# Optimization experiments

Hardware: AMD Instinct MI355X
Metric: run time of the kernel (lower is better)

The kernel has to match this reference:

```python
import jax, jax.numpy as jnp
import numpy as np

NC = 80            # num_classes
REG_MAX = 16
STRIDES = (8, 16, 32)
IMG = 640.0
TOPK = 10
TAL_ALPHA = 0.5
TAL_BETA = 6.0
L_BOX, L_CLS, L_DFL = 7.5, 0.5, 1.5
EPS = 1e-9
NEG = -1e8


def bbox_iou(b1, b2, ciou=False, eps=1e-7):
    # b1, b2: (..., 4) xyxy, broadcastable
    inter_wh = jnp.clip(jnp.minimum(b1[..., 2:], b2[..., 2:]) - jnp.maximum(b1[..., :2], b2[..., :2]), 0.0)
    inter = inter_wh[..., 0] * inter_wh[..., 1]
    w1 = jnp.clip(b1[..., 2] - b1[..., 0], 0.0); h1 = jnp.clip(b1[..., 3] - b1[..., 1], 0.0)
    w2 = jnp.clip(b2[..., 2] - b2[..., 0], 0.0); h2 = jnp.clip(b2[..., 3] - b2[..., 1], 0.0)
    union = w1 * h1 + w2 * h2 - inter + eps
    iou = inter / union
    if not ciou:
        return iou
    cx1 = (b1[..., 0] + b1[..., 2]) * 0.5; cy1 = (b1[..., 1] + b1[..., 3]) * 0.5
    cx2 = (b2[..., 0] + b2[..., 2]) * 0.5; cy2 = (b2[..., 1] + b2[..., 3]) * 0.5
    rho2 = (cx2 - cx1) ** 2 + (cy2 - cy1) ** 2
    cw = jnp.maximum(b1[..., 2], b2[..., 2]) - jnp.minimum(b1[..., 0], b2[..., 0])
    ch = jnp.maximum(b1[..., 3], b2[..., 3]) - jnp.minimum(b1[..., 1], b2[..., 1])
    c2 = cw ** 2 + ch ** 2 + eps
    v = (4.0 / np.pi ** 2) * (jnp.arctan(w2 / (h2 + eps)) - jnp.arctan(w1 / (h1 + eps))) ** 2
    alpha = jax.lax.stop_gradient(v / (1.0 - iou + v + eps))  # torch computes alpha under no_grad
    return iou - (rho2 / c2 + alpha * v)


def _assign_one(pred_scores, pred_bboxes, anchor_points, gt_labels, gt_bboxes):
    """TaskAlignedAssigner for one image.
    pred_scores (N,nc), pred_bboxes (N,4), anchor_points (N,2), gt_labels (M,), gt_bboxes (M,4).
    Returns target_bboxes (N,4), target_scores (N,nc), fg_mask (N,)."""
    N = pred_bboxes.shape[0]; M = gt_bboxes.shape[0]
    gl = jnp.clip(gt_labels.astype(jnp.int32), 0, NC - 1)
    x = anchor_points[:, 0]; y = anchor_points[:, 1]
    l = x[:, None] - gt_bboxes[None, :, 0]
    t = y[:, None] - gt_bboxes[None, :, 1]
    r = gt_bboxes[None, :, 2] - x[:, None]
    b = gt_bboxes[None, :, 3] - y[:, None]
    in_gts = (l > 0) & (t > 0) & (r > 0) & (b > 0)                     # (N,M)
    ious = bbox_iou(pred_bboxes[:, None, :], gt_bboxes[None, :, :])    # (N,M)
    cls_score = pred_scores[:, gl]                                     # (N,M)
    align = jnp.clip(cls_score, 0.0) ** TAL_ALPHA * jnp.clip(ious, 0.0) ** TAL_BETA
    align = jnp.where(in_gts, align, NEG)
    k = min(TOPK, N)
    _, topk_idx = jax.lax.top_k(align.T, k)                            # (M,k) indices into N
    mask_topk = jnp.zeros((M, N), dtype=bool).at[jnp.arange(M)[:, None], topk_idx].set(True).T
    mask_pos = mask_topk & in_gts                                      # (N,M)
    ious_pos = jnp.where(mask_pos, ious, -1.0)
    max_iou = ious_pos.max(axis=1)
    gt_idx = ious_pos.argmax(axis=1)                                   # (N,)
    fg_mask = max_iou > -0.5
    metric_pos = jnp.where(mask_pos, align, NEG)
    metric_max = jnp.clip(metric_pos.max(axis=0), EPS)                 # (M,)
    rows = jnp.arange(N)
    score = align[rows, gt_idx] / metric_max[gt_idx] * ious[rows, gt_idx]
    score = jnp.clip(score, 0.0, 1.0) * fg_mask.astype(pred_scores.dtype)
    tcls = gl[gt_idx]
    target_scores = jnp.zeros((N, NC), dtype=pred_scores.dtype).at[rows, tcls].set(score)
    target_bboxes = jnp.where(fg_mask[:, None], gt_bboxes[gt_idx], 0.0)
    return target_bboxes, target_scores, fg_mask


def _df_loss(reg_logits, target):
    # reg_logits (B,N,4,R) logits, target (B,N,4) float in [0,R-1] -> (B,N)
    t = jnp.clip(target, 0.0, float(REG_MAX - 1))
    left = jnp.floor(t).astype(jnp.int32)
    right = jnp.minimum(left + 1, REG_MAX - 1)
    wl = right.astype(t.dtype) - t
    wr = t - left.astype(t.dtype)
    same = right == left
    wl = jnp.where(same, 1.0, wl)
    wr = jnp.where(same, 0.0, wr)
    logp = jax.nn.log_softmax(reg_logits, axis=-1)
    ll = -jnp.take_along_axis(logp, left[..., None], axis=-1)[..., 0]
    lr = -jnp.take_along_axis(logp, right[..., None], axis=-1)[..., 0]
    return (ll * wl + lr * wr).sum(axis=-1)


def _forward(p0, p1, p2, gt_bboxes, gt_labels):
    preds = [p0, p1, p2]
    B = p0.shape[0]
    reg_ch = 4 * REG_MAX
    cls_list, reg_list, ap_list, st_list = [], [], [], []
    for p, s in zip(preds, STRIDES):
        _, _, h, w = p.shape
        reg = p[:, :reg_ch]
        cls = p[:, reg_ch:]
        cls_list.append(cls.transpose(0, 2, 3, 1).reshape(B, -1, NC))
        reg_list.append(reg.transpose(0, 2, 3, 1).reshape(B, -1, 4, REG_MAX))
        gy, gx = jnp.meshgrid(jnp.arange(h), jnp.arange(w), indexing='ij')
        pts = jnp.stack([(gx + 0.5) * s, (gy + 0.5) * s], axis=-1).reshape(-1, 2).astype(p.dtype)
        ap_list.append(pts)
        st_list.append(jnp.full((h * w,), float(s), dtype=p.dtype))
    cls_logits = jnp.concatenate(cls_list, axis=1)      # (B,N,nc)
    reg_logits = jnp.concatenate(reg_list, axis=1)      # (B,N,4,R)
    anchor_points = jnp.concatenate(ap_list, axis=0)    # (N,2)
    stride_t = jnp.concatenate(st_list, axis=0)         # (N,)
    pred_scores = jax.nn.sigmoid(cls_logits)
    proj = jnp.arange(REG_MAX, dtype=cls_logits.dtype)
    dist = (jax.nn.softmax(reg_logits, axis=-1) * proj).sum(-1) * stride_t[None, :, None]  # (B,N,4)
    ax = anchor_points[:, 0]; ay = anchor_points[:, 1]
    pred_bboxes = jnp.stack([ax - dist[..., 0], ay - dist[..., 1], ax + dist[..., 2], ay + dist[..., 3]], axis=-1)
    # --- TAL assignment (runs under no_grad in torch) ---
    tb, ts, fg = jax.vmap(lambda ps, pb, gl, gb: _assign_one(ps, pb, anchor_points, gl, gb))(
        jax.lax.stop_gradient(pred_scores), jax.lax.stop_gradient(pred_bboxes), gt_labels, gt_bboxes)
    tb = jax.lax.stop_gradient(tb)
    ts = jax.lax.stop_gradient(ts)
    ts_sum = jnp.maximum(ts.sum(), 1.0)
    # --- cls: BCE with logits over all anchors/classes ---
    z = cls_logits
    bce = jnp.clip(z, 0.0) - z * ts + jnp.log1p(jnp.exp(-jnp.abs(z)))
    loss_cls = bce.sum() / ts_sum
    # --- box: CIoU weighted by target score, fg only ---
    weight = ts.sum(-1) * fg.astype(ts.dtype)           # (B,N)
    ciou = bbox_iou(pred_bboxes, tb, ciou=True)         # (B,N)
    loss_box = ((1.0 - ciou) * weight).sum() / ts_sum
    # --- dfl ---
    inv_s = 1.0 / stride_t
    tl = (ax - tb[..., 0]) * inv_s
    tt = (ay - tb[..., 1]) * inv_s
    tr = (tb[..., 2] - ax) * inv_s
    tbm = (tb[..., 3] - ay) * inv_s
    target_ltrb = jnp.clip(jnp.stack([tl, tt, tr, tbm], axis=-1), 0.0, float(REG_MAX - 1))
    dfl = _df_loss(reg_logits, target_ltrb)             # (B,N)
    loss_dfl = (dfl * weight).sum() / ts_sum
    return L_BOX * loss_box + L_CLS * loss_cls + L_DFL * loss_dfl


def setup_inputs() -> dict:
    key = jax.random.key(0)
    k0, k1, k2, kc, kw, kl = jax.random.split(key, 6)
    B, C = 16, 4 * REG_MAX + NC
    p0 = jax.random.normal(k0, (B, C, 80, 80), dtype=jnp.float32)
    p1 = jax.random.normal(k1, (B, C, 40, 40), dtype=jnp.float32)
    p2 = jax.random.normal(k2, (B, C, 20, 20), dtype=jnp.float32)
    M = 32
    cxy = jax.random.uniform(kc, (B, M, 2), minval=64.0, maxval=IMG - 64.0)
    wh = jax.random.uniform(kw, (B, M, 2), minval=16.0, maxval=128.0)
    gt_bboxes = jnp.concatenate([cxy - wh * 0.5, cxy + wh * 0.5], axis=-1).astype(jnp.float32)
    gt_labels = jax.random.randint(kl, (B, M), 0, NC, dtype=jnp.int32).astype(jnp.int64)
    return {"p0": p0, "p1": p1, "p2": p2, "gt_bboxes": gt_bboxes, "gt_labels": gt_labels}


def reference(p0, p1, p2, gt_bboxes, gt_labels):
    return _forward(p0, p1, p2, gt_bboxes, gt_labels)
```

## Files before the change

### kernel.cpp

```cpp
#include <hip/hip_runtime.h>

#define BATCH 16
#define NANCH 8400
#define MGT 32
#define NCLS 80
#define RCH 64
#define NCH 144
#define TOPKK 10
#define MAXC 576
#define TKB 512
#define DECB 2100
#define BCEB 2625
#define TOTB (TKB + DECB + BCEB)
#define FINB 525

struct AInfo { int lvl, pos, W, HW; float s, ax, ay; };

__device__ __forceinline__ AInfo anchor_of(int n) {
  AInfo a;
  if (n < 6400)      { a.lvl = 0; a.pos = n;        a.W = 80; a.HW = 6400; a.s = 8.f;  }
  else if (n < 8000) { a.lvl = 1; a.pos = n - 6400; a.W = 40; a.HW = 1600; a.s = 16.f; }
  else               { a.lvl = 2; a.pos = n - 8000; a.W = 20; a.HW = 400;  a.s = 32.f; }
  int px = a.pos % a.W, py = a.pos / a.W;
  a.ax = (px + 0.5f) * a.s;
  a.ay = (py + 0.5f) * a.s;
  return a;
}

__device__ __forceinline__ const float* lvl_ptr(const float* p0, const float* p1,
                                                const float* p2, int lvl) {
  return lvl == 0 ? p0 : (lvl == 1 ? p1 : p2);
}

__device__ __forceinline__ float4 decode_box(const float* __restrict__ p, size_t chbase,
                                             int HW, float s, float ax, float ay) {
  float d[4];
  #pragma unroll
  for (int q = 0; q < 4; ++q) {
    float z[16]; float zm = -1e30f;
    #pragma unroll
    for (int j = 0; j < 16; ++j) {
      z[j] = p[chbase + (size_t)(q * 16 + j) * HW];
      zm = fmaxf(zm, z[j]);
    }
    float se = 0.f, ae = 0.f;
    #pragma unroll
    for (int j = 0; j < 16; ++j) {
      float e = __expf(z[j] - zm);
      se += e; ae += e * (float)j;
    }
    d[q] = ae / se * s;
  }
  return make_float4(ax - d[0], ay - d[1], ax + d[2], ay + d[3]);
}

__device__ __forceinline__ float iou_xyxy(float4 a, float4 b) {
  float ix = fmaxf(fminf(a.z, b.z) - fmaxf(a.x, b.x), 0.f);
  float iy = fmaxf(fminf(a.w, b.w) - fmaxf(a.y, b.y), 0.f);
  float inter = ix * iy;
  float w1 = fmaxf(a.z - a.x, 0.f), h1 = fmaxf(a.w - a.y, 0.f);
  float w2 = fmaxf(b.z - b.x, 0.f), h2 = fmaxf(b.w - b.y, 0.f);
  float uni = w1 * h1 + w2 * h2 - inter + 1e-7f;
  return inter / uni;
}

__device__ __forceinline__ float ciou_xyxy(float4 a, float4 b) {
  const float eps = 1e-7f;
  float ix = fmaxf(fminf(a.z, b.z) - fmaxf(a.x, b.x), 0.f);
  float iy = fmaxf(fminf(a.w, b.w) - fmaxf(a.y, b.y), 0.f);
  float inter = ix * iy;
  float w1 = fmaxf(a.z - a.x, 0.f), h1 = fmaxf(a.w - a.y, 0.f);
  float w2 = fmaxf(b.z - b.x, 0.f), h2 = fmaxf(b.w - b.y, 0.f);
  float uni = w1 * h1 + w2 * h2 - inter + eps;
  float iou = inter / uni;
  float cx1 = (a.x + a.z) * 0.5f, cy1 = (a.y + a.w) * 0.5f;
  float cx2 = (b.x + b.z) * 0.5f, cy2 = (b.y + b.w) * 0.5f;
  float rho2 = (cx2 - cx1) * (cx2 - cx1) + (cy2 - cy1) * (cy2 - cy1);
  float cw = fmaxf(a.z, b.z) - fminf(a.x, b.x);
  float ch = fmaxf(a.w, b.w) - fminf(a.y, b.y);
  float c2 = cw * cw + ch * ch + eps;
  const float kpi = 4.f / (float)(M_PI * M_PI);
  float dat = atanf(w2 / (h2 + eps)) - atanf(w1 / (h1 + eps));
  float v = kpi * dat * dat;
  float alpha = v / (1.f - iou + v + eps);
  return iou - (rho2 / c2 + alpha * v);
}

__device__ __forceinline__ float block_sum256(float v) {
  __shared__ float sm[4];
  #pragma unroll
  for (int off = 32; off; off >>= 1) v += __shfl_xor(v, off);
  __syncthreads();
  if ((threadIdx.x & 63) == 0) sm[threadIdx.x >> 6] = v;
  __syncthreads();
  return (threadIdx.x == 0) ? (sm[0] + sm[1] + sm[2] + sm[3]) : 0.f;
}

__device__ __forceinline__ double block_sum256d(double v) {
  __shared__ double smd[4];
  #pragma unroll
  for (int off = 32; off; off >>= 1) v += __shfl_xor(v, off);
  __syncthreads();
  if ((threadIdx.x & 63) == 0) smd[threadIdx.x >> 6] = v;
  __syncthreads();
  return (threadIdx.x == 0) ? (smd[0] + smd[1] + smd[2] + smd[3]) : 0.0;
}

__global__ __launch_bounds__(256) void k_one(
    const float* __restrict__ p0, const float* __restrict__ p1, const float* __restrict__ p2,
    const float* __restrict__ gtb, const int* __restrict__ gtl,
    float* __restrict__ pboxf, float* __restrict__ logz,
    float* __restrict__ metric_max, unsigned long long* __restrict__ slots,
    float* __restrict__ bce_part) {
  __shared__ float val[MAXC];
  __shared__ int   idx[MAXC];
  __shared__ float cio[MAXC];
  __shared__ float rv[4];
  __shared__ int   ri[4], rs[4], sdone[1];
  int blk = blockIdx.x, tid = threadIdx.x;

  if (blk >= TKB + DECB) {
    int r = blk - (TKB + DECB);
    int i = r * 256 + tid;
    float lb = 0.f;
    #pragma unroll
    for (int j = 0; j < 4; ++j) {
      int u = i + j * 672000;
      int b = u / 168000;
      int rr = u % 168000;
      const float4* src;
      if (rr < 128000)      src = (const float4*)p0 + ((size_t)(b * NCH + RCH) * 1600 + rr);
      else if (rr < 160000) src = (const float4*)p1 + ((size_t)(b * NCH + RCH) * 400 + (rr - 128000));
      else                  src = (const float4*)p2 + ((size_t)(b * NCH + RCH) * 100 + (rr - 160000));
      float4 z4 = *src;
      lb += fmaxf(z4.x, 0.f) + __logf(1.f + __expf(-fabsf(z4.x)));
      lb += fmaxf(z4.y, 0.f) + __logf(1.f + __expf(-fabsf(z4.y)));
      lb += fmaxf(z4.z, 0.f) + __logf(1.f + __expf(-fabsf(z4.z)));
      lb += fmaxf(z4.w, 0.f) + __logf(1.f + __expf(-fabsf(z4.w)));
    }
    float tot = block_sum256(lb);
    if (tid == 0) bce_part[r] = tot;
    return;
  }

  if (blk >= TKB) {
    int db = blk - TKB;
    int q = db & 3;
    int i = (db >> 2) * 256 + tid;
    int b = i / NANCH, n = i % NANCH;
    AInfo A = anchor_of(n);
    const float* p = lvl_ptr(p0, p1, p2, A.lvl);
    size_t base = (size_t)b * NCH * A.HW + A.pos;

    float z[16]; float zm = -1e30f;
    #pragma unroll
    for (int j = 0; j < 16; ++j) {
      z[j] = p[base + (size_t)(q * 16 + j) * A.HW];
      zm = fmaxf(zm, z[j]);
    }
    float se = 0.f, ae = 0.f;
    #pragma unroll
    for (int j = 0; j < 16; ++j) {
      float e = __expf(z[j] - zm);
      se += e; ae += e * (float)j;
    }
    float d = ae / se * A.s;
    float v = (q == 0) ? A.ax - d : (q == 1) ? A.ay - d : (q == 2) ? A.ax + d : A.ay + d;
    pboxf[(size_t)i * 4 + q] = v;
    logz[(size_t)i * 4 + q] = zm + __logf(se);
    return;
  }

  int b = blk >> 5, m = blk & 31;
  float4 g = ((const float4*)gtb)[b * MGT + m];
  int gl = min(max(gtl[b * MGT + m], 0), NCLS - 1);

  const int   Ws[3] = {80, 40, 20};
  const float ss[3] = {8.f, 16.f, 32.f};
  const int   nb[3] = {0, 6400, 8000};
  int x0[3], y0[3], nxl[3], cb[3];
  int cnt = 0;
  #pragma unroll
  for (int L = 0; L < 3; ++L) {
    float s = ss[L]; int W = Ws[L];
    int ax0 = max((int)floorf(g.x / s - 0.5f), 0);
    int ax1 = min((int)ceilf (g.z / s - 0.5f), W - 1);
    int ay0 = max((int)floorf(g.y / s - 0.5f), 0);
    int ay1 = min((int)ceilf (g.w / s - 0.5f), W - 1);
    int nx = max(ax1 - ax0 + 1, 0);
    int ny = max(ay1 - ay0 + 1, 0);
    x0[L] = ax0; y0[L] = ay0; nxl[L] = nx;
    cb[L] = cnt; cnt += nx * ny;
  }
  int C = min(cnt, MAXC);

  for (int t = tid; t < C; t += 256) {
    int L = (t >= cb[2]) ? 2 : (t >= cb[1]) ? 1 : 0;
    int r = t - cb[L];
    int ix = r % nxl[L], iy = r / nxl[L];
    int px = x0[L] + ix, py = y0[L] + iy;
    float ax = (px + 0.5f) * ss[L], ay = (py + 0.5f) * ss[L];
    float al = -3e38f, iou = 0.f; int n = 0x7fffffff;
    if (ax > g.x && ay > g.y && ax < g.z && ay < g.w) {
      int W = Ws[L];
      int HW = (L == 0) ? 6400 : (L == 1) ? 1600 : 400;
      int pos = py * W + px;
      n = nb[L] + pos;
      const float* p = lvl_ptr(p0, p1, p2, L);
      size_t chbase = (size_t)b * NCH * HW + pos;
      float4 pb = decode_box(p, chbase, HW, ss[L], ax, ay);
      iou = iou_xyxy(pb, g);
      float z = p[chbase + (size_t)(RCH + gl) * HW];
      float sg = 1.f / (1.f + __expf(-z));
      float i3 = iou * iou * iou;
      al = sqrtf(sg) * i3 * i3;
    }
    val[t] = al; idx[t] = n; cio[t] = iou;
  }
  __syncthreads();

  float mmax = -1.f;
  for (int k = 0; k < TOPKK; ++k) {
    float bv = -3e38f; int bn = 0x7fffffff, bs = 0;
    for (int t = tid; t < C; t += 256) {
      float v = val[t]; int n2 = idx[t];
      if (v > bv || (v == bv && n2 < bn)) { bv = v; bn = n2; bs = t; }
    }
    #pragma unroll
    for (int off = 32; off; off >>= 1) {
      float ov = __shfl_xor(bv, off);
      int   on = __shfl_xor(bn, off);
      int   os = __shfl_xor(bs, off);
      if (ov > bv || (ov == bv && on < bn)) { bv = ov; bn = on; bs = os; }
    }
    if ((tid & 63) == 0) { rv[tid >> 6] = bv; ri[tid >> 6] = bn; rs[tid >> 6] = bs; }
    __syncthreads();
    if (tid == 0) {
      #pragma unroll
      for (int w = 1; w < 4; ++w)
        if (rv[w] > bv || (rv[w] == bv && ri[w] < bn)) { bv = rv[w]; bn = ri[w]; bs = rs[w]; }
      if (bv >= 0.f) {
        mmax = fmaxf(mmax, bv);
        unsigned long long key = (1ULL << 62) |
                                 ((unsigned long long)__float_as_uint(cio[bs]) << 6) |
                                 (unsigned long long)(31 - m);
        atomicMax(&slots[(size_t)b * NANCH + bn], key);
        val[bs] = -3e38f;
        sdone[0] = 0;
      } else sdone[0] = 1;
    }
    __syncthreads();
    if (sdone[0]) break;
  }
  if (tid == 0) metric_max[b * MGT + m] = fmaxf(mmax, 1e-9f);
}

__global__ __launch_bounds__(256) void k_fin(
    const float* __restrict__ p0, const float* __restrict__ p1, const float* __restrict__ p2,
    const float4* __restrict__ pbox, const float* __restrict__ logz,
    const float* __restrict__ gtb, const int* __restrict__ gtl,
    const float* __restrict__ metric_max, const unsigned long long* __restrict__ slots,
    float4* __restrict__ fin_part) {
  int i = blockIdx.x * 256 + threadIdx.x;
  unsigned long long key = slots[i];
  float ts_p = 0.f, zc_p = 0.f, box_p = 0.f, dfl_p = 0.f;
  if (key) {
    int b = i / NANCH, n = i % NANCH;
    int m = 31 - (int)(key & 63ULL);
    float iou = __uint_as_float((unsigned int)((key >> 6) & 0xFFFFFFFFULL));
    AInfo A = anchor_of(n);
    float4 g = ((const float4*)gtb)[b * MGT + m];
    int gl = min(max(gtl[b * MGT + m], 0), NCLS - 1);
    const float* p = lvl_ptr(p0, p1, p2, A.lvl);
    size_t base = (size_t)b * NCH * A.HW + A.pos;

    float z = p[base + (size_t)(RCH + gl) * A.HW];
    float sg = 1.f / (1.f + __expf(-z));
    float i3 = iou * iou * iou;
    float align = sqrtf(sg) * i3 * i3;
    float mm = metric_max[b * MGT + m];
    float score = fminf(fmaxf(align / mm * iou, 0.f), 1.f);

    ts_p = score;
    zc_p = z * score;

    float4 pb = pbox[i];
    float ciou = ciou_xyxy(pb, g);
    box_p = (1.f - ciou) * score;

    float4 lz4 = ((const float4*)logz)[i];
    float inv_s = 1.f / A.s;
    float targ0 = (A.ax - g.x) * inv_s;
    float targ1 = (A.ay - g.y) * inv_s;
    float targ2 = (g.z - A.ax) * inv_s;
    float targ3 = (g.w - A.ay) * inv_s;
    float dfl = 0.f;
    #pragma unroll
    for (int sd = 0; sd < 4; ++sd) {
      float tg = sd == 0 ? targ0 : sd == 1 ? targ1 : sd == 2 ? targ2 : targ3;
      float lZ = sd == 0 ? lz4.x : sd == 1 ? lz4.y : sd == 2 ? lz4.z : lz4.w;
      float t = fminf(fmaxf(tg, 0.f), 15.f);
      int left = (int)floorf(t);
      int right = min(left + 1, 15);
      float wl, wr;
      if (right == left) { wl = 1.f; wr = 0.f; }
      else               { wl = (float)right - t; wr = t - (float)left; }
      float zl = p[base + (size_t)(sd * 16 + left)  * A.HW];
      float zr = p[base + (size_t)(sd * 16 + right) * A.HW];
      dfl += wl * (lZ - zl) + wr * (lZ - zr);
    }
    dfl_p = dfl * score;
  }
  float s0 = block_sum256(box_p);
  float s1 = block_sum256(zc_p);
  float s2 = block_sum256(dfl_p);
  float s3 = block_sum256(ts_p);
  if (threadIdx.x == 0) fin_part[blockIdx.x] = make_float4(s0, s1, s2, s3);
}

__global__ void k_out(const float* __restrict__ bce_part, const float4* __restrict__ fin_part,
                      float* __restrict__ out) {
  int tid = threadIdx.x;
  double sb = 0.0, s0 = 0.0, s1 = 0.0, s2 = 0.0, s3 = 0.0;
  for (int t = tid; t < BCEB; t += 256) sb += (double)bce_part[t];
  for (int t = tid; t < FINB; t += 256) {
    float4 f = fin_part[t];
    s0 += (double)f.x; s1 += (double)f.y; s2 += (double)f.z; s3 += (double)f.w;
  }
  sb = block_sum256d(sb);
  s0 = block_sum256d(s0);
  s1 = block_sum256d(s1);
  s2 = block_sum256d(s2);
  s3 = block_sum256d(s3);
  if (tid == 0) {
    double ts = fmax(s3, 1.0);
    out[0] = (float)(7.5 * s0 / ts + 0.5 * (sb - s1) / ts + 1.5 * s2 / ts);
  }
}

extern "C" void kernel_launch(void* const* d_in, const int* in_sizes, int n_in,
                              void* d_out, int out_size, void* d_ws, size_t ws_size,
                              hipStream_t stream) {
  const float* p0  = (const float*)d_in[0];
  const float* p1  = (const float*)d_in[1];
  const float* p2  = (const float*)d_in[2];
  const float* gtb = (const float*)d_in[3];
  const int*   gtl = (const int*)d_in[4];
  float* out = (float*)d_out;

  char* ws = (char*)d_ws;
  float*  metric_max = (float*)ws;
  float*  bce_part   = (float*)(ws + 2048);
  float4* fin_part   = (float4*)(ws + 12560);
  float*  pboxf      = (float*)(ws + 20960);
  float4* pbox       = (float4*)(ws + 20960);
  float*  logz       = (float*)(ws + 2171360);
  unsigned long long* slots = (unsigned long long*)(ws + 4321760);

  hipMemsetAsync(slots, 0, (size_t)BATCH * NANCH * 8, stream);
  k_one<<<TOTB, 256, 0, stream>>>(p0, p1, p2, gtb, gtl, pboxf, logz,
                                  metric_max, slots, bce_part);
  k_fin<<<FINB, 256, 0, stream>>>(p0, p1, p2, pbox, logz, gtb, gtl,
                                  metric_max, slots, fin_part);
  k_out<<<1, 256, 0, stream>>>(bce_part, fin_part, out);
}
```

Measured before the change: 135.3 us.

## Decode DFL boxes only for foreground anchors inside the final kernel

Removes the dense decode pass that computed softmax-expected box distances and log-partition values for every anchor and wrote them to workspace. The final kernel now recomputes these only for anchors that received an assignment, reading all 64 regression logits per foreground anchor. This drops a large read of the regression channels plus the pbox/logz writes and reads. In exchange, foreground threads do more gathered loads, and warps are divergent because only some lanes are foreground.

```diff
diff --git a/kernel.cpp b/kernel.cpp
--- a/kernel.cpp
+++ b/kernel.cpp
@@ -9,9 +9,8 @@
 #define TOPKK 10
 #define MAXC 576
 #define TKB 512
-#define DECB 2100
 #define BCEB 2625
-#define TOTB (TKB + DECB + BCEB)
+#define TOTB (TKB + BCEB)
 #define FINB 525
 
 struct AInfo { int lvl, pos, W, HW; float s, ax, ay; };
@@ -109,7 +108,6 @@
 __global__ __launch_bounds__(256) void k_one(
     const float* __restrict__ p0, const float* __restrict__ p1, const float* __restrict__ p2,
     const float* __restrict__ gtb, const int* __restrict__ gtl,
-    float* __restrict__ pboxf, float* __restrict__ logz,
     float* __restrict__ metric_max, unsigned long long* __restrict__ slots,
     float* __restrict__ bce_part) {
   __shared__ float val[MAXC];
@@ -119,8 +117,8 @@
   __shared__ int   ri[4], rs[4], sdone[1];
   int blk = blockIdx.x, tid = threadIdx.x;
 
-  if (blk >= TKB + DECB) {
-    int r = blk - (TKB + DECB);
+  if (blk >= TKB) {
+    int r = blk - TKB;
     int i = r * 256 + tid;
     float lb = 0.f;
     #pragma unroll
@@ -140,34 +138,6 @@
     }
     float tot = block_sum256(lb);
     if (tid == 0) bce_part[r] = tot;
-    return;
-  }
-
-  if (blk >= TKB) {
-    int db = blk - TKB;
-    int q = db & 3;
-    int i = (db >> 2) * 256 + tid;
-    int b = i / NANCH, n = i % NANCH;
-    AInfo A = anchor_of(n);
-    const float* p = lvl_ptr(p0, p1, p2, A.lvl);
-    size_t base = (size_t)b * NCH * A.HW + A.pos;
-
-    float z[16]; float zm = -1e30f;
-    #pragma unroll
-    for (int j = 0; j < 16; ++j) {
-      z[j] = p[base + (size_t)(q * 16 + j) * A.HW];
-      zm = fmaxf(zm, z[j]);
-    }
-    float se = 0.f, ae = 0.f;
-    #pragma unroll
-    for (int j = 0; j < 16; ++j) {
-      float e = __expf(z[j] - zm);
-      se += e; ae += e * (float)j;
-    }
-    float d = ae / se * A.s;
-    float v = (q == 0) ? A.ax - d : (q == 1) ? A.ay - d : (q == 2) ? A.ax + d : A.ay + d;
-    pboxf[(size_t)i * 4 + q] = v;
-    logz[(size_t)i * 4 + q] = zm + __logf(se);
     return;
   }
 
@@ -257,7 +227,6 @@
 
 __global__ __launch_bounds__(256) void k_fin(
     const float* __restrict__ p0, const float* __restrict__ p1, const float* __restrict__ p2,
-    const float4* __restrict__ pbox, const float* __restrict__ logz,
     const float* __restrict__ gtb, const int* __restrict__ gtl,
     const float* __restrict__ metric_max, const unsigned long long* __restrict__ slots,
     float4* __restrict__ fin_part) {
@@ -284,32 +253,45 @@
     ts_p = score;
     zc_p = z * score;
 
-    float4 pb = pbox[i];
-    float ciou = ciou_xyxy(pb, g);
-    box_p = (1.f - ciou) * score;
-
-    float4 lz4 = ((const float4*)logz)[i];
     float inv_s = 1.f / A.s;
     float targ0 = (A.ax - g.x) * inv_s;
     float targ1 = (A.ay - g.y) * inv_s;
     float targ2 = (g.z - A.ax) * inv_s;
     float targ3 = (g.w - A.ay) * inv_s;
-    float dfl = 0.f;
+
+    float d[4]; float dfl = 0.f;
     #pragma unroll
     for (int sd = 0; sd < 4; ++sd) {
       float tg = sd == 0 ? targ0 : sd == 1 ? targ1 : sd == 2 ? targ2 : targ3;
-      float lZ = sd == 0 ? lz4.x : sd == 1 ? lz4.y : sd == 2 ? lz4.z : lz4.w;
       float t = fminf(fmaxf(tg, 0.f), 15.f);
       int left = (int)floorf(t);
       int right = min(left + 1, 15);
       float wl, wr;
       if (right == left) { wl = 1.f; wr = 0.f; }
       else               { wl = (float)right - t; wr = t - (float)left; }
-      float zl = p[base + (size_t)(sd * 16 + left)  * A.HW];
-      float zr = p[base + (size_t)(sd * 16 + right) * A.HW];
-      dfl += wl * (lZ - zl) + wr * (lZ - zr);
+      float zz[16]; float zm = -1e30f;
+      #pragma unroll
+      for (int j = 0; j < 16; ++j) {
+        zz[j] = p[base + (size_t)(sd * 16 + j) * A.HW];
+        zm = fmaxf(zm, zz[j]);
+      }
+      float se = 0.f, ae = 0.f, zl = 0.f, zr = 0.f;
+      #pragma unroll
+      for (int j = 0; j < 16; ++j) {
+        float e = __expf(zz[j] - zm);
+        se += e; ae += e * (float)j;
+        if (j == left)  zl = zz[j];
+        if (j == right) zr = zz[j];
+      }
+      d[sd] = ae / se * A.s;
+      float logZ = zm + __logf(se);
+      dfl += wl * (logZ - zl) + wr * (logZ - zr);
     }
     dfl_p = dfl * score;
+
+    float4 pb = make_float4(A.ax - d[0], A.ay - d[1], A.ax + d[2], A.ay + d[3]);
+    float ciou = ciou_xyxy(pb, g);
+    box_p = (1.f - ciou) * score;
   }
   float s0 = block_sum256(box_p);
   float s1 = block_sum256(zc_p);
@@ -352,15 +334,10 @@
   float*  metric_max = (float*)ws;
   float*  bce_part   = (float*)(ws + 2048);
   float4* fin_part   = (float4*)(ws + 12560);
-  float*  pboxf      = (float*)(ws + 20960);
-  float4* pbox       = (float4*)(ws + 20960);
-  float*  logz       = (float*)(ws + 2171360);
-  unsigned long long* slots = (unsigned long long*)(ws + 4321760);
+  unsigned long long* slots = (unsigned long long*)(ws + 20960);
 
   hipMemsetAsync(slots, 0, (size_t)BATCH * NANCH * 8, stream);
-  k_one<<<TOTB, 256, 0, stream>>>(p0, p1, p2, gtb, gtl, pboxf, logz,
-                                  metric_max, slots, bce_part);
-  k_fin<<<FINB, 256, 0, stream>>>(p0, p1, p2, pbox, logz, gtb, gtl,
-                                  metric_max, slots, fin_part);
+  k_one<<<TOTB, 256, 0, stream>>>(p0, p1, p2, gtb, gtl, metric_max, slots, bce_part);
+  k_fin<<<FINB, 256, 0, stream>>>(p0, p1, p2, gtb, gtl, metric_max, slots, fin_part);
   k_out<<<1, 256, 0, stream>>>(bce_part, fin_part, out);
 }
```

After: 137.3 us. Within noise of the previous version (+1.4%).
